# Kernel optimization log

Hardware: AMD Instinct MI355X
Metric: run time of the kernel (lower is better)

The kernel has to match this reference:

```python
import jax, jax.numpy as jnp
import numpy as np

N = 50000       # nodes
E = 1_600_000   # edges (before self-loops)
IN = 128        # in_channels
OUT = 32        # out_channels per head
H = 2           # heads
NEG_SLOPE = 0.2 # PyG GATConv default leaky-relu slope


def setup_inputs() -> dict:
    key = jax.random.key(0)
    k = jax.random.split(key, 6)
    x = jax.random.normal(k[0], (N, IN), jnp.float32)
    edge_index = jax.random.randint(k[1], (2, E), 0, N, dtype=jnp.int64)
    W = jax.random.normal(k[2], (IN, H * OUT), jnp.float32) / np.sqrt(IN).astype(np.float32)
    att_src = jax.random.normal(k[3], (H, OUT), jnp.float32) * 0.1
    att_dst = jax.random.normal(k[4], (H, OUT), jnp.float32) * 0.1
    bias = jax.random.normal(k[5], (H * OUT,), jnp.float32) * 0.01
    return {"x": x, "edge_index": edge_index, "W": W,
            "att_src": att_src, "att_dst": att_dst, "bias": bias}


def reference(x, edge_index, W, att_src, att_dst, bias):
    n = x.shape[0]
    h_, c = att_src.shape
    # add self-loops (PyG GATConv default add_self_loops=True)
    loops = jnp.arange(n, dtype=edge_index.dtype)
    src = jnp.concatenate([edge_index[0], loops])  # [E+N]
    dst = jnp.concatenate([edge_index[1], loops])  # [E+N]
    # linear transform -> [N, H, C]
    h = (x @ W).reshape(n, h_, c)
    # per-node attention logits per head
    a_src = jnp.einsum('nhc,hc->nh', h, att_src)  # [N, H]
    a_dst = jnp.einsum('nhc,hc->nh', h, att_dst)  # [N, H]
    # per-edge scores
    e = jax.nn.leaky_relu(a_src[src] + a_dst[dst], NEG_SLOPE)  # [E+N, H]
    # segment softmax over incoming edges of each dst node
    seg_max = jax.ops.segment_max(e, dst, num_segments=n)      # [N, H]
    ex = jnp.exp(e - seg_max[dst])
    denom = jax.ops.segment_sum(ex, dst, num_segments=n)       # [N, H]
    alpha = ex / denom[dst]                                    # [E+N, H]
    # weighted scatter-aggregate of source features
    msg = alpha[:, :, None] * h[src]                           # [E+N, H, C]
    out = jax.ops.segment_sum(msg, dst, num_segments=n)        # [N, H, C]
    return out.reshape(n, h_ * c) + bias
```

## Files before the change

### kernel.cpp

```cpp
#include <hip/hip_runtime.h>
#include <hip/hip_fp16.h>

#define N_NODES 50000
#define N_EDGES 1600000
#define IN_CH   128
#define NEG     0.2f
#define NBUK    391
#define BCAP    4608
#define CAP     80
#define CHUNK   4096
#define P_BLOCKS 391
#define PT      512

static __device__ __forceinline__ __half2 u2h2(unsigned u) {
    union { unsigned u; __half2 h; } x; x.u = u; return x.h;
}

__global__ __launch_bounds__(256) void gemm_logits(
    const float* __restrict__ x, const float* __restrict__ W,
    const float* __restrict__ att_src, const float* __restrict__ att_dst,
    unsigned int* __restrict__ hI, float* __restrict__ as_, float* __restrict__ ad_,
    int* __restrict__ gcur)
{
    if (blockIdx.x == 0) {
        for (int i = threadIdx.x; i < NBUK; i += 256) gcur[i] = 0;
    }

    __shared__ float Wl[IN_CH * 64];
    for (int i = threadIdx.x; i < IN_CH * 64; i += 256) Wl[i] = W[i];
    __syncthreads();

    int gid = blockIdx.x * 256 + threadIdx.x;
    int row = gid >> 2;
    int sub = gid & 3;
    if (row >= N_NODES) return;

    float acc[16];
#pragma unroll
    for (int c = 0; c < 16; ++c) acc[c] = 0.f;

    const float* xr = x + (size_t)row * IN_CH;
    for (int k = 0; k < IN_CH; k += 4) {
        float4 xv = *(const float4*)(xr + k);
        float xs[4] = {xv.x, xv.y, xv.z, xv.w};
#pragma unroll
        for (int kk = 0; kk < 4; ++kk) {
            const float* wr = &Wl[(k + kk) * 64 + sub * 16];
#pragma unroll
            for (int c = 0; c < 16; c += 4) {
                float4 wv = *(const float4*)(wr + c);
                acc[c]     += xs[kk] * wv.x;
                acc[c + 1] += xs[kk] * wv.y;
                acc[c + 2] += xs[kk] * wv.z;
                acc[c + 3] += xs[kk] * wv.w;
            }
        }
    }

    float part[16];
#pragma unroll
    for (int i = 0; i < 16; ++i) part[i] = __shfl_xor(acc[i], 2);

    if (sub < 2) {
        union { unsigned int u[16]; uint4 v4[4]; } pk;
#pragma unroll
        for (int i = 0; i < 16; ++i) {
            pk.u[i] = (unsigned)__half_as_ushort(__float2half_rn(acc[i])) |
                      ((unsigned)__half_as_ushort(__float2half_rn(part[i])) << 16);
        }
        uint4* hp = (uint4*)(hI + (size_t)row * 32 + sub * 16);
#pragma unroll
        for (int i = 0; i < 4; ++i) hp[i] = pk.v4[i];
    }

    float s = 0.f, d = 0.f;
#pragma unroll
    for (int c = 0; c < 16; ++c) {
        s += acc[c] * att_src[sub * 16 + c];
        d += acc[c] * att_dst[sub * 16 + c];
    }
    s += __shfl_xor(s, 1);
    d += __shfl_xor(d, 1);
    if ((sub & 1) == 0) {
        as_[row * 2 + (sub >> 1)] = s;
        ad_[row * 2 + (sub >> 1)] = d;
    }
}

__global__ __launch_bounds__(PT) void partition(
    const int* __restrict__ ei, int* __restrict__ gcur,
    unsigned int* __restrict__ barr)
{
    __shared__ int hist[NBUK];
    __shared__ int start[NBUK];
    __shared__ int gbase[NBUK];
    __shared__ int lofs[NBUK];
    __shared__ int wsum[8];
    __shared__ int woff[8];
    __shared__ unsigned int buf[CHUNK];

    int tid = threadIdx.x;
    int lane = tid & 63, wid = tid >> 6;
    int cbase = blockIdx.x * CHUNK;
    int cnt = N_EDGES - cbase;
    if (cnt > CHUNK) cnt = CHUNK;
    int n4 = cnt >> 2;

    for (int i = tid; i < NBUK; i += PT) { hist[i] = 0; lofs[i] = 0; }
    __syncthreads();

    const int4* s4 = (const int4*)ei + (cbase >> 2);
    const int4* d4 = (const int4*)(ei + N_EDGES) + (cbase >> 2);

    int4 dv[2], sv[2];
#pragma unroll
    for (int i = 0; i < 2; ++i) {
        int k = i * PT + tid;
        if (k < n4) {
            dv[i] = d4[k]; sv[i] = s4[k];
            atomicAdd(&hist[dv[i].x >> 7], 1);
            atomicAdd(&hist[dv[i].y >> 7], 1);
            atomicAdd(&hist[dv[i].z >> 7], 1);
            atomicAdd(&hist[dv[i].w >> 7], 1);
        }
    }
    __syncthreads();

    int a = (tid < NBUK) ? hist[tid] : 0;
    int orig = a;
#pragma unroll
    for (int off = 1; off < 64; off <<= 1) {
        int u = __shfl_up(a, off);
        if (lane >= off) a += u;
    }
    if (lane == 63) wsum[wid] = a;
    __syncthreads();
    if (tid == 0) {
        int r = 0;
#pragma unroll
        for (int w = 0; w < 8; ++w) { woff[w] = r; r += wsum[w]; }
    }
    __syncthreads();
    a += woff[wid];
    if (tid < NBUK) {
        start[tid] = a - orig;
        gbase[tid] = atomicAdd(&gcur[tid], orig);
    }
    __syncthreads();

#pragma unroll
    for (int i = 0; i < 2; ++i) {
        int k = i * PT + tid;
        if (k < n4) {
            int dd[4] = {dv[i].x, dv[i].y, dv[i].z, dv[i].w};
            int ss[4] = {sv[i].x, sv[i].y, sv[i].z, sv[i].w};
#pragma unroll
            for (int e = 0; e < 4; ++e) {
                int d = dd[e];
                int bkt = d >> 7;
                int loc = atomicAdd(&lofs[bkt], 1);
                buf[start[bkt] + loc] =
                    (unsigned)ss[e] | ((unsigned)(d & 127) << 16) | ((unsigned)bkt << 23);
            }
        }
    }
    __syncthreads();

    for (int i = tid; i < cnt; i += PT) {
        unsigned u = buf[i];
        int bkt = u >> 23;
        int g = gbase[bkt] + (i - start[bkt]);
        if (g < BCAP) barr[(size_t)bkt * BCAP + g] = u & 0x7FFFFFu;
    }
}

__global__ __launch_bounds__(512) void aggregate(
    const unsigned int* __restrict__ hI, const float* __restrict__ as_,
    const float* __restrict__ ad_, const int* __restrict__ gcur,
    const unsigned int* __restrict__ barr, const float* __restrict__ bias,
    float* __restrict__ out)
{
    __shared__ unsigned short lcol[32 * CAP];
    __shared__ int hist[32];

    int b     = blockIdx.x >> 2;
    int jbase = (blockIdx.x & 3) << 5;
    int tid   = threadIdx.x;
    if (tid < 32) hist[tid] = 0;
    __syncthreads();

    int cnt = gcur[b];
    if (cnt > BCAP) cnt = BCAP;
    const unsigned int* bb = barr + (size_t)b * BCAP;

    for (int i = tid; i < cnt; i += 512) {
        unsigned u = bb[i];
        int r = ((int)(u >> 16) & 127) - jbase;
        if ((unsigned)r < 32u) {
            int k = atomicAdd(&hist[r], 1);
            if (k < CAP) lcol[r * CAP + k] = (unsigned short)(u & 0xFFFFu);
        }
    }
    __syncthreads();

    int lane = tid & 63;
    int wave = tid >> 6;
    int c    = lane & 31;
    int hv   = lane >> 5;
    int sl   = lane & 32;
    float bi0 = bias[c], bi1 = bias[32 + c];

    for (int pass = 0; pass < 2; ++pass) {
        int r = pass * 16 + (wave << 1) + hv;
        int node = b * 128 + jbase + r;
        bool valid = (node < N_NODES);

        float2 adv = valid ? *(const float2*)(ad_ + node * 2) : make_float2(0.f, 0.f);
        float2 asv = valid ? *(const float2*)(as_ + node * 2) : make_float2(0.f, 0.f);

        float t0 = asv.x + adv.x, t1 = asv.y + adv.y;
        float e0 = (t0 > 0.f) ? t0 : NEG * t0;
        float e1 = (t1 > 0.f) ? t1 : NEG * t1;
        float p0s = __expf(e0), p1s = __expf(e1);
        unsigned hs = valid ? hI[(unsigned)node * 32u + c] : 0u;
        __half2 hsh = u2h2(hs);
        float self0 = p0s * __half2float(__low2half(hsh));
        float self1 = p1s * __half2float(__high2half(hsh));
        float s0 = 0.f, s1 = 0.f;

        __half2 z = __float2half2_rn(0.f);
        __half2 acA = z, acB = z, acC = z, acD = z;

        int n = valid ? min(hist[r], CAP) : 0;
        const unsigned short* cb = &lcol[r * CAP];
        int nmax = max(n, __shfl_xor(n, 32));

        for (int base = 0; base < nmax; base += 32) {
            unsigned msrc = 0, packP = 0;
            int myidx = base + c;
            if (myidx < n) {
                int srci = (int)cb[myidx];
                float2 av = *(const float2*)(as_ + srci * 2);
                float u0 = av.x + adv.x, u1 = av.y + adv.y;
                float f0 = (u0 > 0.f) ? u0 : NEG * u0;
                float f1 = (u1 > 0.f) ? u1 : NEG * u1;
                float q0 = __expf(f0), q1 = __expf(f1);
                s0 += q0; s1 += q1;
                msrc  = (unsigned)srci;
                packP = (unsigned)__half_as_ushort(__float2half_rn(q0)) |
                        ((unsigned)__half_as_ushort(__float2half_rn(q1)) << 16);
            }
            int c32 = nmax - base;
            if (c32 > 32) c32 = 32;

            int jj = 0;
            for (; jj + 8 <= c32; jj += 8) {
                unsigned sA = __shfl(msrc, sl + jj);
                unsigned sB = __shfl(msrc, sl + jj + 1);
                unsigned sC = __shfl(msrc, sl + jj + 2);
                unsigned sD = __shfl(msrc, sl + jj + 3);
                unsigned sE = __shfl(msrc, sl + jj + 4);
                unsigned sF = __shfl(msrc, sl + jj + 5);
                unsigned sG = __shfl(msrc, sl + jj + 6);
                unsigned sH = __shfl(msrc, sl + jj + 7);
                unsigned pA = __shfl(packP, sl + jj);
                unsigned pB = __shfl(packP, sl + jj + 1);
                unsigned pC = __shfl(packP, sl + jj + 2);
                unsigned pD = __shfl(packP, sl + jj + 3);
                unsigned pE = __shfl(packP, sl + jj + 4);
                unsigned pF = __shfl(packP, sl + jj + 5);
                unsigned pG = __shfl(packP, sl + jj + 6);
                unsigned pH = __shfl(packP, sl + jj + 7);
                unsigned vA = hI[sA * 32u + c];
                unsigned vB = hI[sB * 32u + c];
                unsigned vC = hI[sC * 32u + c];
                unsigned vD = hI[sD * 32u + c];
                unsigned vE = hI[sE * 32u + c];
                unsigned vF = hI[sF * 32u + c];
                unsigned vG = hI[sG * 32u + c];
                unsigned vH = hI[sH * 32u + c];
                acA = __hfma2(u2h2(vA), u2h2(pA), acA);
                acB = __hfma2(u2h2(vB), u2h2(pB), acB);
                acC = __hfma2(u2h2(vC), u2h2(pC), acC);
                acD = __hfma2(u2h2(vD), u2h2(pD), acD);
                acA = __hfma2(u2h2(vE), u2h2(pE), acA);
                acB = __hfma2(u2h2(vF), u2h2(pF), acB);
                acC = __hfma2(u2h2(vG), u2h2(pG), acC);
                acD = __hfma2(u2h2(vH), u2h2(pH), acD);
            }
            for (; jj < c32; ++jj) {
                unsigned sA = __shfl(msrc, sl + jj);
                unsigned pA = __shfl(packP, sl + jj);
                unsigned vA = hI[sA * 32u + c];
                acA = __hfma2(u2h2(vA), u2h2(pA), acA);
            }
        }

        float2 fA = __half22float2(acA);
        float2 fB = __half22float2(acB);
        float2 fC = __half22float2(acC);
        float2 fD = __half22float2(acD);
        float acc0 = (fA.x + fB.x) + (fC.x + fD.x) + self0;
        float acc1 = (fA.y + fB.y) + (fC.y + fD.y) + self1;

        s0 += __shfl_xor(s0, 16); s1 += __shfl_xor(s1, 16);
        s0 += __shfl_xor(s0, 8);  s1 += __shfl_xor(s1, 8);
        s0 += __shfl_xor(s0, 4);  s1 += __shfl_xor(s1, 4);
        s0 += __shfl_xor(s0, 2);  s1 += __shfl_xor(s1, 2);
        s0 += __shfl_xor(s0, 1);  s1 += __shfl_xor(s1, 1);
        s0 += p0s; s1 += p1s;

        if (valid) {
            out[(size_t)node * 64 + c]      = acc0 / s0 + bi0;
            out[(size_t)node * 64 + 32 + c] = acc1 / s1 + bi1;
        }
    }
}

extern "C" void kernel_launch(void* const* d_in, const int* in_sizes, int n_in,
                              void* d_out, int out_size, void* d_ws, size_t ws_size,
                              hipStream_t stream)
{
    const float* x       = (const float*)d_in[0];
    const int*   ei      = (const int*)d_in[1];
    const float* W       = (const float*)d_in[2];
    const float* att_src = (const float*)d_in[3];
    const float* att_dst = (const float*)d_in[4];
    const float* bias    = (const float*)d_in[5];
    float* out = (float*)d_out;

    char* ws = (char*)d_ws;
    size_t off = 0;
    auto alloc = [&](size_t bytes) -> void* {
        void* p = ws + off;
        off = (off + bytes + 511) & ~(size_t)511;
        return p;
    };
    unsigned int* hI  = (unsigned int*)alloc((size_t)N_NODES * 32 * 4);
    float*  as_ = (float*)alloc((size_t)N_NODES * 2 * 4);
    float*  ad_ = (float*)alloc((size_t)N_NODES * 2 * 4);
    int*    gcur = (int*)alloc((size_t)NBUK * 4);
    unsigned int* barr = (unsigned int*)alloc((size_t)NBUK * BCAP * 4);

    gemm_logits<<<(N_NODES * 4 + 255) / 256, 256, 0, stream>>>(
        x, W, att_src, att_dst, hI, as_, ad_, gcur);
    partition<<<P_BLOCKS, PT, 0, stream>>>(ei, gcur, barr);
    aggregate<<<NBUK * 4, 512, 0, stream>>>(hI, as_, ad_, gcur, barr, bias, out);
}
```

Baseline: 81.45 us.

## Shrink destination buckets to 32 nodes so aggregate blocks read only their own edges

Destination buckets shrink from 128 nodes to 32 nodes (1563 buckets). Each aggregate block now owns exactly one bucket instead of four blocks each scanning a shared 128-node bucket and discarding three quarters of the entries. The partition kernel grows its shared histogram to 2048 entries and scans four buckets per thread, and it skips the global atomic for empty buckets. The trade-off is more global atomics on the bucket cursors, more scattered small writes into the bucket arrays, and more shared memory in partition, which may lower its occupancy.

Result: slower. 102.5 us (+25.9%).

```diff
diff --git a/kernel.cpp b/kernel.cpp
--- a/kernel.cpp
+++ b/kernel.cpp
@@ -5,8 +5,9 @@
 #define N_EDGES 1600000
 #define IN_CH   128
 #define NEG     0.2f
-#define NBUK    391
-#define BCAP    4608
+#define NBUK    1563
+#define PBUK    2048
+#define BCAP    1280
 #define CAP     80
 #define CHUNK   4096
 #define P_BLOCKS 391
@@ -91,10 +92,10 @@
     const int* __restrict__ ei, int* __restrict__ gcur,
     unsigned int* __restrict__ barr)
 {
-    __shared__ int hist[NBUK];
-    __shared__ int start[NBUK];
-    __shared__ int gbase[NBUK];
-    __shared__ int lofs[NBUK];
+    __shared__ int hist[PBUK];
+    __shared__ int start[PBUK];
+    __shared__ int gbase[PBUK];
+    __shared__ int lofs[PBUK];
     __shared__ int wsum[8];
     __shared__ int woff[8];
     __shared__ unsigned int buf[CHUNK];
@@ -106,7 +107,7 @@
     if (cnt > CHUNK) cnt = CHUNK;
     int n4 = cnt >> 2;
 
-    for (int i = tid; i < NBUK; i += PT) { hist[i] = 0; lofs[i] = 0; }
+    for (int i = tid; i < PBUK; i += PT) { hist[i] = 0; lofs[i] = 0; }
     __syncthreads();
 
     const int4* s4 = (const int4*)ei + (cbase >> 2);
@@ -118,16 +119,18 @@
         int k = i * PT + tid;
         if (k < n4) {
             dv[i] = d4[k]; sv[i] = s4[k];
-            atomicAdd(&hist[dv[i].x >> 7], 1);
-            atomicAdd(&hist[dv[i].y >> 7], 1);
-            atomicAdd(&hist[dv[i].z >> 7], 1);
-            atomicAdd(&hist[dv[i].w >> 7], 1);
-        }
-    }
-    __syncthreads();
-
-    int a = (tid < NBUK) ? hist[tid] : 0;
-    int orig = a;
+            atomicAdd(&hist[dv[i].x >> 5], 1);
+            atomicAdd(&hist[dv[i].y >> 5], 1);
+            atomicAdd(&hist[dv[i].z >> 5], 1);
+            atomicAdd(&hist[dv[i].w >> 5], 1);
+        }
+    }
+    __syncthreads();
+
+    int b0 = tid << 2;
+    int h0 = hist[b0], h1 = hist[b0 + 1], h2 = hist[b0 + 2], h3 = hist[b0 + 3];
+    int tsum = h0 + h1 + h2 + h3;
+    int a = tsum;
 #pragma unroll
     for (int off = 1; off < 64; off <<= 1) {
         int u = __shfl_up(a, off);
@@ -141,10 +144,16 @@
         for (int w = 0; w < 8; ++w) { woff[w] = r; r += wsum[w]; }
     }
     __syncthreads();
-    a += woff[wid];
-    if (tid < NBUK) {
-        start[tid] = a - orig;
-        gbase[tid] = atomicAdd(&gcur[tid], orig);
+    int run = a - tsum + woff[wid];
+    start[b0] = run;
+    start[b0 + 1] = run + h0;
+    start[b0 + 2] = run + h0 + h1;
+    start[b0 + 3] = run + h0 + h1 + h2;
+    if (b0 < NBUK) {
+        if (h0 > 0) gbase[b0] = atomicAdd(&gcur[b0], h0);
+        if (b0 + 1 < NBUK && h1 > 0) gbase[b0 + 1] = atomicAdd(&gcur[b0 + 1], h1);
+        if (b0 + 2 < NBUK && h2 > 0) gbase[b0 + 2] = atomicAdd(&gcur[b0 + 2], h2);
+        if (b0 + 3 < NBUK && h3 > 0) gbase[b0 + 3] = atomicAdd(&gcur[b0 + 3], h3);
     }
     __syncthreads();
 
@@ -157,10 +166,10 @@
 #pragma unroll
             for (int e = 0; e < 4; ++e) {
                 int d = dd[e];
-                int bkt = d >> 7;
+                int bkt = d >> 5;
                 int loc = atomicAdd(&lofs[bkt], 1);
                 buf[start[bkt] + loc] =
-                    (unsigned)ss[e] | ((unsigned)(d & 127) << 16) | ((unsigned)bkt << 23);
+                    (unsigned)ss[e] | ((unsigned)(d & 31) << 16) | ((unsigned)bkt << 21);
             }
         }
     }
@@ -168,9 +177,9 @@
 
     for (int i = tid; i < cnt; i += PT) {
         unsigned u = buf[i];
-        int bkt = u >> 23;
+        int bkt = u >> 21;
         int g = gbase[bkt] + (i - start[bkt]);
-        if (g < BCAP) barr[(size_t)bkt * BCAP + g] = u & 0x7FFFFFu;
+        if (g < BCAP) barr[(size_t)bkt * BCAP + g] = u & 0x1FFFFFu;
     }
 }
 
@@ -183,9 +192,8 @@
     __shared__ unsigned short lcol[32 * CAP];
     __shared__ int hist[32];
 
-    int b     = blockIdx.x >> 2;
-    int jbase = (blockIdx.x & 3) << 5;
-    int tid   = threadIdx.x;
+    int b   = blockIdx.x;
+    int tid = threadIdx.x;
     if (tid < 32) hist[tid] = 0;
     __syncthreads();
 
@@ -195,11 +203,9 @@
 
     for (int i = tid; i < cnt; i += 512) {
         unsigned u = bb[i];
-        int r = ((int)(u >> 16) & 127) - jbase;
-        if ((unsigned)r < 32u) {
-            int k = atomicAdd(&hist[r], 1);
-            if (k < CAP) lcol[r * CAP + k] = (unsigned short)(u & 0xFFFFu);
-        }
+        int r = (int)(u >> 16) & 31;
+        int k = atomicAdd(&hist[r], 1);
+        if (k < CAP) lcol[r * CAP + k] = (unsigned short)(u & 0xFFFFu);
     }
     __syncthreads();
 
@@ -212,7 +218,7 @@
 
     for (int pass = 0; pass < 2; ++pass) {
         int r = pass * 16 + (wave << 1) + hv;
-        int node = b * 128 + jbase + r;
+        int node = b * 32 + r;
         bool valid = (node < N_NODES);
 
         float2 adv = valid ? *(const float2*)(ad_ + node * 2) : make_float2(0.f, 0.f);
@@ -345,5 +351,5 @@
     gemm_logits<<<(N_NODES * 4 + 255) / 256, 256, 0, stream>>>(
         x, W, att_src, att_dst, hI, as_, ad_, gcur);
     partition<<<P_BLOCKS, PT, 0, stream>>>(ei, gcur, barr);
-    aggregate<<<NBUK * 4, 512, 0, stream>>>(hI, as_, ad_, gcur, barr, bias, out);
-}
+    aggregate<<<NBUK, 512, 0, stream>>>(hI, as_, ad_, gcur, barr, bias, out);
+}
```
